# Optimization experiments

Hardware: AMD Instinct MI355X
Metric: run time of the kernel (lower is better)

## Reference

```python
import jax, jax.numpy as jnp
import numpy as np

B, H, S, DK = 2, 16, 2048, 64


def setup_inputs() -> dict:
    key = jax.random.key(0)
    kq, kk, kv = jax.random.split(key, 3)
    query = jax.random.normal(kq, (B, H, S, DK), dtype=jnp.float32)
    k = jax.random.normal(kk, (B, H, S, DK), dtype=jnp.float32)
    value = jax.random.normal(kv, (B, H, S, DK), dtype=jnp.float32)
    # causal padding-style mask: 1 = keep, 0 = masked (set to -inf pre-softmax)
    mask = jnp.tril(jnp.ones((S, S), dtype=jnp.int32))[None, None, :, :]
    return {"query": query, "key": k, "value": value, "d_k": DK, "mask": mask}


def reference(query, key, value, d_k, mask):
    # scores: [B, H, Sq, Sk]
    scores = jnp.einsum("bhqd,bhkd->bhqk", query, key)
    scores = scores / jnp.sqrt(jnp.asarray(d_k, dtype=scores.dtype))
    scores = jnp.where(mask == 0, -jnp.inf, scores)
    att = jax.nn.softmax(scores, axis=-1)
    # dropout is identity in eval mode (deterministic reference)
    out = jnp.einsum("bhqk,bhkd->bhqd", att, value)
    return out
```

## Files before the change

### kernel.cpp

```cpp
#include <hip/hip_runtime.h>
#include <cstdint>

#define B_ 2
#define H_ 16
#define S_ 2048
#define DK_ 64
#define BH_ (B_*H_)
#define NQT 32

typedef __attribute__((ext_vector_type(8))) short short8;
typedef __attribute__((ext_vector_type(4))) short short4v;
typedef __attribute__((ext_vector_type(4))) float floatx4;

__device__ inline unsigned short f2bf(float f) {
  union { float f; unsigned u; } v; v.f = f;
  unsigned u = v.u;
  unsigned r = u + 0x7fffu + ((u >> 16) & 1u);
  return (unsigned short)(r >> 16);
}

__device__ inline floatx4 mfma16(short4v a, short4v b, floatx4 c) {
#if __has_builtin(__builtin_amdgcn_mfma_f32_16x16x16bf16_1k)
  return __builtin_amdgcn_mfma_f32_16x16x16bf16_1k(a, b, c, 0, 0, 0);
#else
  asm("v_mfma_f32_16x16x16_bf16 %0, %1, %2, %0" : "+v"(c) : "v"(a), "v"(b));
  return c;
#endif
}

__device__ inline short4v u2s4(unsigned a, unsigned b) {
  union { unsigned u[2]; short4v s; } v;
  v.u[0] = a; v.u[1] = b;
  return v.s;
}

__global__ __launch_bounds__(256) void conv_kv(const float* __restrict__ K,
                                               const float* __restrict__ V,
                                               unsigned short* __restrict__ Kb,
                                               unsigned short* __restrict__ Vb) {
  __shared__ __align__(16) unsigned short t[64 * 80];
  const int bh = blockIdx.y, s0 = blockIdx.x * 64;
  const int row = threadIdx.x >> 2, cp = threadIdx.x & 3;

  {
    const float* src = K + ((size_t)(bh * S_ + s0 + row)) * DK_ + cp * 16;
    unsigned short* dst = Kb + ((size_t)(bh * S_ + s0 + row)) * DK_ + cp * 16;
    #pragma unroll
    for (int h = 0; h < 2; ++h) {
      float4 a = *(const float4*)(src + h * 8);
      float4 b = *(const float4*)(src + h * 8 + 4);
      uint4 st;
      st.x = (unsigned)f2bf(a.x) | ((unsigned)f2bf(a.y) << 16);
      st.y = (unsigned)f2bf(a.z) | ((unsigned)f2bf(a.w) << 16);
      st.z = (unsigned)f2bf(b.x) | ((unsigned)f2bf(b.y) << 16);
      st.w = (unsigned)f2bf(b.z) | ((unsigned)f2bf(b.w) << 16);
      *(uint4*)(dst + h * 8) = st;
    }
  }
  {
    const float* src = V + ((size_t)(bh * S_ + s0 + row)) * DK_ + cp * 16;
    #pragma unroll
    for (int j4 = 0; j4 < 4; ++j4) {
      float4 a = *(const float4*)(src + j4 * 4);
      int c = cp * 16 + j4 * 4;
      t[(c + 0) * 80 + row] = f2bf(a.x);
      t[(c + 1) * 80 + row] = f2bf(a.y);
      t[(c + 2) * 80 + row] = f2bf(a.z);
      t[(c + 3) * 80 + row] = f2bf(a.w);
    }
    __syncthreads();
    unsigned short* dst = Vb + ((size_t)(bh * DK_ + row)) * S_ + s0 + cp * 16;
    #pragma unroll
    for (int g = 0; g < 2; ++g) {
      const int pg = 2 * cp + g;
      const int t2r = pg >> 2, q = pg & 3;
      uint2 a = *(const uint2*)&t[row * 80 + 32 * t2r + 4 * q];
      uint2 b = *(const uint2*)&t[row * 80 + 32 * t2r + 16 + 4 * q];
      uint4 st = {a.x, a.y, b.x, b.y};
      *(uint4*)(dst + g * 8) = st;
    }
  }
}

__global__ __launch_bounds__(256, 2)
void fa_kernel(const float* __restrict__ Q, const unsigned short* __restrict__ Kb,
               const unsigned short* __restrict__ Vb, float* __restrict__ Out) {
  __shared__ __align__(16) unsigned short Kt[8192];
  __shared__ __align__(16) unsigned short Vt[8192];

  const int tid  = threadIdx.x;
  const int wave = tid >> 6;
  const int lane = tid & 63;
  const int quad = lane >> 4;
  const int l16  = lane & 15;
  const int wq   = wave & 1;
  const int ws   = wave >> 1;

  const int id = blockIdx.x;
  const int bh = (id & 7) | (((id >> 3) & 3) << 3);
  const int qt = NQT - 1 - (id >> 5);

  const float SCL = 0.125f * 1.44269504088896340736f;

  short8 qf[4];
  #pragma unroll
  for (int nq = 0; nq < 2; ++nq) {
    const float* p = Q + ((size_t)bh * S_ + qt * 64 + wq * 32 + nq * 16 + l16) * DK_ + quad * 8;
    #pragma unroll
    for (int ks = 0; ks < 2; ++ks) {
      float4 x = *(const float4*)(p + ks * 32);
      float4 y = *(const float4*)(p + ks * 32 + 4);
      short8 t;
      t[0]=(short)f2bf(x.x*SCL); t[1]=(short)f2bf(x.y*SCL); t[2]=(short)f2bf(x.z*SCL); t[3]=(short)f2bf(x.w*SCL);
      t[4]=(short)f2bf(y.x*SCL); t[5]=(short)f2bf(y.y*SCL); t[6]=(short)f2bf(y.z*SCL); t[7]=(short)f2bf(y.w*SCL);
      qf[nq * 2 + ks] = t;
    }
  }

  floatx4 Ot[4][2];
  float ls[2] = {0.f, 0.f};
  #pragma unroll
  for (int d = 0; d < 4; ++d)
    #pragma unroll
    for (int nq = 0; nq < 2; ++nq) Ot[d][nq] = (floatx4){0,0,0,0};

  const int nkv = (qt >> 1) + 1;
  for (int kv = 0; kv < nkv; ++kv) {
    if (kv) __syncthreads();
    #pragma unroll
    for (int rd = 0; rd < 4; ++rd) {
      const int cid = rd * 256 + wave * 64 + lane;
      {
        int row = cid >> 3, p = cid & 7, c = p ^ (row & 7);
        const unsigned short* g = Kb + (((size_t)bh * S_ + kv * 128 + row) << 6) + (c << 3);
        __builtin_amdgcn_global_load_lds(
            (const __attribute__((address_space(1))) void*)g,
            (__attribute__((address_space(3))) void*)&Kt[(rd * 4 + wave) * 512], 16, 0, 0);
      }
      {
        int row = cid >> 4, p = cid & 15, c = p ^ (row & 15);
        const unsigned short* g = Vb + (((size_t)bh * DK_ + row) << 11) + kv * 128 + (c << 3);
        __builtin_amdgcn_global_load_lds(
            (const __attribute__((address_space(1))) void*)g,
            (__attribute__((address_space(3))) void*)&Vt[(rd * 4 + wave) * 512], 16, 0, 0);
      }
    }
    __syncthreads();

    const bool domask = (kv == nkv - 1);
    unsigned pk[4][2][2];
    #pragma unroll
    for (int nt = 0; nt < 4; ++nt) {
      const int row = ws * 64 + nt * 16 + l16;
      floatx4 s0 = (floatx4){0,0,0,0}, s1 = (floatx4){0,0,0,0};
      #pragma unroll
      for (int ks = 0; ks < 2; ++ks) {
        const int p = (ks * 4 + quad) ^ (row & 7);
        const short8 ak = *(const short8*)&Kt[row * 64 + p * 8];
        s0 = __builtin_amdgcn_mfma_f32_16x16x32_bf16(ak, qf[ks],     s0, 0, 0, 0);
        s1 = __builtin_amdgcn_mfma_f32_16x16x32_bf16(ak, qf[2 + ks], s1, 0, 0, 0);
      }
      if (domask) {
        const int sb  = kv * 128 + ws * 64 + nt * 16 + quad * 4;
        const int q0r = qt * 64 + wq * 32 + l16;
        #pragma unroll
        for (int r = 0; r < 4; ++r) {
          if (sb + r > q0r)      s0[r] = -INFINITY;
          if (sb + r > q0r + 16) s1[r] = -INFINITY;
        }
      }
      #pragma unroll
      for (int nq = 0; nq < 2; ++nq) {
        const floatx4 sv = nq ? s1 : s0;
        float e0 = __builtin_amdgcn_exp2f(sv[0]);
        float e1 = __builtin_amdgcn_exp2f(sv[1]);
        float e2 = __builtin_amdgcn_exp2f(sv[2]);
        float e3 = __builtin_amdgcn_exp2f(sv[3]);
        ls[nq] += (e0 + e1) + (e2 + e3);
        pk[nt][nq][0] = __builtin_amdgcn_perm(__float_as_uint(e1) + 0x8000u,
                                              __float_as_uint(e0) + 0x8000u, 0x07060302u);
        pk[nt][nq][1] = __builtin_amdgcn_perm(__float_as_uint(e3) + 0x8000u,
                                              __float_as_uint(e2) + 0x8000u, 0x07060302u);
      }
    }
    #pragma unroll
    for (int dblk = 0; dblk < 4; ++dblk) {
      const int row = dblk * 16 + l16;
      #pragma unroll
      for (int tt = 0; tt < 2; ++tt) {
        const int p = ((ws * 2 + tt) * 4 + quad) ^ l16;
        const short8 v8 = *(const short8*)&Vt[row * 128 + p * 8];
        const short4v vlo = __builtin_shufflevector(v8, v8, 0, 1, 2, 3);
        const short4v vhi = __builtin_shufflevector(v8, v8, 4, 5, 6, 7);
        #pragma unroll
        for (int nq = 0; nq < 2; ++nq) {
          Ot[dblk][nq] = mfma16(vlo, u2s4(pk[2*tt  ][nq][0], pk[2*tt  ][nq][1]), Ot[dblk][nq]);
          Ot[dblk][nq] = mfma16(vhi, u2s4(pk[2*tt+1][nq][0], pk[2*tt+1][nq][1]), Ot[dblk][nq]);
        }
      }
    }
  }
  __syncthreads();

  #pragma unroll
  for (int nq = 0; nq < 2; ++nq) {
    ls[nq] += __shfl_xor(ls[nq], 16);
    ls[nq] += __shfl_xor(ls[nq], 32);
  }
  float* OP = (float*)&Kt[0];
  float* LP = (float*)&Vt[0];
  if (ws == 1) {
    #pragma unroll
    for (int nq = 0; nq < 2; ++nq) {
      const int rowi = (wq * 2 + nq) * 16 + l16;
      #pragma unroll
      for (int dblk = 0; dblk < 4; ++dblk) {
        const int c2 = (dblk * 4 + quad) ^ (l16 & 12);
        *(floatx4*)&OP[rowi * 64 + c2 * 4] = Ot[dblk][nq];
      }
      if (quad == 0) LP[rowi] = ls[nq];
    }
  }
  __syncthreads();
  if (ws == 0) {
    #pragma unroll
    for (int nq = 0; nq < 2; ++nq) {
      const int rowi = (wq * 2 + nq) * 16 + l16;
      const float inv = 1.0f / (ls[nq] + LP[rowi]);
      float* og = Out + ((size_t)bh * S_ + qt * 64 + wq * 32 + nq * 16 + l16) * DK_;
      #pragma unroll
      for (int dblk = 0; dblk < 4; ++dblk) {
        const int c2 = (dblk * 4 + quad) ^ (l16 & 12);
        floatx4 tot = Ot[dblk][nq] + *(const floatx4*)&OP[rowi * 64 + c2 * 4];
        tot *= inv;
        *(floatx4*)(og + dblk * 16 + quad * 4) = tot;
      }
    }
  }
}

extern "C" void kernel_launch(void* const* d_in, const int* in_sizes, int n_in,
                              void* d_out, int out_size, void* d_ws, size_t ws_size,
                              hipStream_t stream) {
  const float* Q = (const float*)d_in[0];
  const float* K = (const float*)d_in[1];
  const float* V = (const float*)d_in[2];
  float* Out = (float*)d_out;
  unsigned short* Kb = (unsigned short*)d_ws;
  unsigned short* Vb = Kb + (size_t)BH_ * S_ * DK_;
  conv_kv<<<dim3(S_ / 64, BH_), 256, 0, stream>>>(K, V, Kb, Vb);
  fa_kernel<<<dim3(NQT * BH_), 256, 0, stream>>>(Q, Kb, Vb, Out);
}
```

Before: 140.6 us.

## Replace 4-wave LDS-tiled attention blocks with single-wave blocks reading K/V directly

Each block becomes one wavefront handling a 32-row query strip, loading K and V fragments straight from global memory instead of staging 128-key tiles into shared memory. This removes the LDS staging, the barriers and the cross-wave reduction of partial outputs. The grid grows to 2048 small blocks for finer load balancing across the causal workload. In exchange K/V reuse across query waves now depends on L2/L1 caching, and there is no prefetch overlap.

```diff
diff --git a/kernel.cpp b/kernel.cpp
--- a/kernel.cpp
+++ b/kernel.cpp
@@ -6,7 +6,6 @@
 #define S_ 2048
 #define DK_ 64
 #define BH_ (B_*H_)
-#define NQT 32
 
 typedef __attribute__((ext_vector_type(8))) short short8;
 typedef __attribute__((ext_vector_type(4))) short short4v;
@@ -82,30 +81,22 @@
   }
 }
 
-__global__ __launch_bounds__(256, 2)
+__global__ __launch_bounds__(64, 3)
 void fa_kernel(const float* __restrict__ Q, const unsigned short* __restrict__ Kb,
                const unsigned short* __restrict__ Vb, float* __restrict__ Out) {
-  __shared__ __align__(16) unsigned short Kt[8192];
-  __shared__ __align__(16) unsigned short Vt[8192];
-
-  const int tid  = threadIdx.x;
-  const int wave = tid >> 6;
-  const int lane = tid & 63;
+  const int lane = threadIdx.x;
   const int quad = lane >> 4;
   const int l16  = lane & 15;
-  const int wq   = wave & 1;
-  const int ws   = wave >> 1;
-
-  const int id = blockIdx.x;
-  const int bh = (id & 7) | (((id >> 3) & 3) << 3);
-  const int qt = NQT - 1 - (id >> 5);
+  const int id   = blockIdx.x;
+  const int bh   = id & 31;
+  const int strip = 63 - (id >> 5);
 
   const float SCL = 0.125f * 1.44269504088896340736f;
 
   short8 qf[4];
   #pragma unroll
   for (int nq = 0; nq < 2; ++nq) {
-    const float* p = Q + ((size_t)bh * S_ + qt * 64 + wq * 32 + nq * 16 + l16) * DK_ + quad * 8;
+    const float* p = Q + ((size_t)bh * S_ + strip * 32 + nq * 16 + l16) * DK_ + quad * 8;
     #pragma unroll
     for (int ks = 0; ks < 2; ++ks) {
       float4 x = *(const float4*)(p + ks * 32);
@@ -124,54 +115,37 @@
     #pragma unroll
     for (int nq = 0; nq < 2; ++nq) Ot[d][nq] = (floatx4){0,0,0,0};
 
-  const int nkv = (qt >> 1) + 1;
-  for (int kv = 0; kv < nkv; ++kv) {
-    if (kv) __syncthreads();
-    #pragma unroll
-    for (int rd = 0; rd < 4; ++rd) {
-      const int cid = rd * 256 + wave * 64 + lane;
-      {
-        int row = cid >> 3, p = cid & 7, c = p ^ (row & 7);
-        const unsigned short* g = Kb + (((size_t)bh * S_ + kv * 128 + row) << 6) + (c << 3);
-        __builtin_amdgcn_global_load_lds(
-            (const __attribute__((address_space(1))) void*)g,
-            (__attribute__((address_space(3))) void*)&Kt[(rd * 4 + wave) * 512], 16, 0, 0);
-      }
-      {
-        int row = cid >> 4, p = cid & 15, c = p ^ (row & 15);
-        const unsigned short* g = Vb + (((size_t)bh * DK_ + row) << 11) + kv * 128 + (c << 3);
-        __builtin_amdgcn_global_load_lds(
-            (const __attribute__((address_space(1))) void*)g,
-            (__attribute__((address_space(3))) void*)&Vt[(rd * 4 + wave) * 512], 16, 0, 0);
-      }
-    }
-    __syncthreads();
-
-    const bool domask = (kv == nkv - 1);
+  const unsigned short* Kbase = Kb + (size_t)bh * S_ * DK_;
+  const unsigned short* Vbase = Vb + (size_t)bh * DK_ * S_;
+
+  const int niter = (strip >> 1) + 1;
+
+  for (int it = 0; it < niter; ++it) {
+    const int s0 = it * 64;
+    const bool dm = (it == niter - 1);
     unsigned pk[4][2][2];
+
     #pragma unroll
     for (int nt = 0; nt < 4; ++nt) {
-      const int row = ws * 64 + nt * 16 + l16;
-      floatx4 s0 = (floatx4){0,0,0,0}, s1 = (floatx4){0,0,0,0};
+      floatx4 a0 = (floatx4){0,0,0,0}, a1 = (floatx4){0,0,0,0};
       #pragma unroll
       for (int ks = 0; ks < 2; ++ks) {
-        const int p = (ks * 4 + quad) ^ (row & 7);
-        const short8 ak = *(const short8*)&Kt[row * 64 + p * 8];
-        s0 = __builtin_amdgcn_mfma_f32_16x16x32_bf16(ak, qf[ks],     s0, 0, 0, 0);
-        s1 = __builtin_amdgcn_mfma_f32_16x16x32_bf16(ak, qf[2 + ks], s1, 0, 0, 0);
-      }
-      if (domask) {
-        const int sb  = kv * 128 + ws * 64 + nt * 16 + quad * 4;
-        const int q0r = qt * 64 + wq * 32 + l16;
+        const short8 kf = *(const short8*)(Kbase + (size_t)(s0 + nt * 16 + l16) * DK_ + ks * 32 + quad * 8);
+        a0 = __builtin_amdgcn_mfma_f32_16x16x32_bf16(kf, qf[ks],     a0, 0, 0, 0);
+        a1 = __builtin_amdgcn_mfma_f32_16x16x32_bf16(kf, qf[2 + ks], a1, 0, 0, 0);
+      }
+      if (dm) {
+        const int sg = s0 + nt * 16 + quad * 4;
+        const int q0 = strip * 32 + l16;
         #pragma unroll
         for (int r = 0; r < 4; ++r) {
-          if (sb + r > q0r)      s0[r] = -INFINITY;
-          if (sb + r > q0r + 16) s1[r] = -INFINITY;
+          if (sg + r > q0)      a0[r] = -INFINITY;
+          if (sg + r > q0 + 16) a1[r] = -INFINITY;
         }
       }
       #pragma unroll
       for (int nq = 0; nq < 2; ++nq) {
-        const floatx4 sv = nq ? s1 : s0;
+        const floatx4 sv = nq ? a1 : a0;
         float e0 = __builtin_amdgcn_exp2f(sv[0]);
         float e1 = __builtin_amdgcn_exp2f(sv[1]);
         float e2 = __builtin_amdgcn_exp2f(sv[2]);
@@ -183,13 +157,13 @@
                                               __float_as_uint(e2) + 0x8000u, 0x07060302u);
       }
     }
+
     #pragma unroll
     for (int dblk = 0; dblk < 4; ++dblk) {
-      const int row = dblk * 16 + l16;
+      const unsigned short* vp = Vbase + (size_t)(dblk * 16 + l16) * S_ + s0 + quad * 8;
       #pragma unroll
       for (int tt = 0; tt < 2; ++tt) {
-        const int p = ((ws * 2 + tt) * 4 + quad) ^ l16;
-        const short8 v8 = *(const short8*)&Vt[row * 128 + p * 8];
+        const short8 v8 = *(const short8*)(vp + tt * 32);
         const short4v vlo = __builtin_shufflevector(v8, v8, 0, 1, 2, 3);
         const short4v vhi = __builtin_shufflevector(v8, v8, 4, 5, 6, 7);
         #pragma unroll
@@ -200,41 +174,20 @@
       }
     }
   }
-  __syncthreads();
 
   #pragma unroll
   for (int nq = 0; nq < 2; ++nq) {
     ls[nq] += __shfl_xor(ls[nq], 16);
     ls[nq] += __shfl_xor(ls[nq], 32);
   }
-  float* OP = (float*)&Kt[0];
-  float* LP = (float*)&Vt[0];
-  if (ws == 1) {
-    #pragma unroll
-    for (int nq = 0; nq < 2; ++nq) {
-      const int rowi = (wq * 2 + nq) * 16 + l16;
-      #pragma unroll
-      for (int dblk = 0; dblk < 4; ++dblk) {
-        const int c2 = (dblk * 4 + quad) ^ (l16 & 12);
-        *(floatx4*)&OP[rowi * 64 + c2 * 4] = Ot[dblk][nq];
-      }
-      if (quad == 0) LP[rowi] = ls[nq];
-    }
-  }
-  __syncthreads();
-  if (ws == 0) {
-    #pragma unroll
-    for (int nq = 0; nq < 2; ++nq) {
-      const int rowi = (wq * 2 + nq) * 16 + l16;
-      const float inv = 1.0f / (ls[nq] + LP[rowi]);
-      float* og = Out + ((size_t)bh * S_ + qt * 64 + wq * 32 + nq * 16 + l16) * DK_;
-      #pragma unroll
-      for (int dblk = 0; dblk < 4; ++dblk) {
-        const int c2 = (dblk * 4 + quad) ^ (l16 & 12);
-        floatx4 tot = Ot[dblk][nq] + *(const floatx4*)&OP[rowi * 64 + c2 * 4];
-        tot *= inv;
-        *(floatx4*)(og + dblk * 16 + quad * 4) = tot;
-      }
+  #pragma unroll
+  for (int nq = 0; nq < 2; ++nq) {
+    const float inv = 1.0f / ls[nq];
+    float* og = Out + ((size_t)bh * S_ + strip * 32 + nq * 16 + l16) * DK_;
+    #pragma unroll
+    for (int dblk = 0; dblk < 4; ++dblk) {
+      floatx4 tot = Ot[dblk][nq] * inv;
+      *(floatx4*)(og + dblk * 16 + quad * 4) = tot;
     }
   }
 }
@@ -249,5 +202,5 @@
   unsigned short* Kb = (unsigned short*)d_ws;
   unsigned short* Vb = Kb + (size_t)BH_ * S_ * DK_;
   conv_kv<<<dim3(S_ / 64, BH_), 256, 0, stream>>>(K, V, Kb, Vb);
-  fa_kernel<<<dim3(NQT * BH_), 256, 0, stream>>>(Q, Kb, Vb, Out);
-}
+  fa_kernel<<<dim3(64 * BH_), 64, 0, stream>>>(Q, Kb, Vb, Out);
+}
```

New measurement: 207.0 us. +47.2%, slower.

## Double-buffer K tiles in LDS and load V fragments directly into registers

Applied to the files above, without the earlier changes.

K tiles are now double-buffered in shared memory, and the next tile is prefetched asynchronously while the current one is computed, so each iteration needs only one barrier. V no longer goes through shared memory. Each wave reads its V fragments straight from global memory into registers at the start of the iteration. This hides load latency behind the MFMA work, at the cost of more registers and uncoalesced 16-byte global V loads that are exposed if the cache misses.

```diff
diff --git a/kernel.cpp b/kernel.cpp
--- a/kernel.cpp
+++ b/kernel.cpp
@@ -85,8 +85,7 @@
 __global__ __launch_bounds__(256, 2)
 void fa_kernel(const float* __restrict__ Q, const unsigned short* __restrict__ Kb,
                const unsigned short* __restrict__ Vb, float* __restrict__ Out) {
-  __shared__ __align__(16) unsigned short Kt[8192];
-  __shared__ __align__(16) unsigned short Vt[8192];
+  __shared__ __align__(16) unsigned short Kt[2][8192];
 
   const int tid  = threadIdx.x;
   const int wave = tid >> 6;
@@ -124,54 +123,69 @@
     #pragma unroll
     for (int nq = 0; nq < 2; ++nq) Ot[d][nq] = (floatx4){0,0,0,0};
 
+  const unsigned short* Kbase = Kb + (size_t)bh * S_ * DK_;
+  const unsigned short* Vbase = Vb + (size_t)bh * DK_ * S_ + ws * 64 + quad * 8;
+
+  int lofs[4];
+  #pragma unroll
+  for (int rd = 0; rd < 4; ++rd) {
+    const int cid = rd * 256 + wave * 64 + lane;
+    const int row = cid >> 3, p = cid & 7, c = p ^ (row & 7);
+    lofs[rd] = row * 64 + c * 8;
+  }
+
+  auto stageK = [&](int buf, int kv) {
+    #pragma unroll
+    for (int rd = 0; rd < 4; ++rd) {
+      const unsigned short* g = Kbase + kv * (128 * DK_) + lofs[rd];
+      __builtin_amdgcn_global_load_lds(
+          (const __attribute__((address_space(1))) void*)g,
+          (__attribute__((address_space(3))) void*)&Kt[buf][(rd * 4 + wave) * 512], 16, 0, 0);
+    }
+  };
+
   const int nkv = (qt >> 1) + 1;
+  stageK(0, 0);
+  __syncthreads();
+
+  int cur = 0;
   for (int kv = 0; kv < nkv; ++kv) {
-    if (kv) __syncthreads();
-    #pragma unroll
-    for (int rd = 0; rd < 4; ++rd) {
-      const int cid = rd * 256 + wave * 64 + lane;
-      {
-        int row = cid >> 3, p = cid & 7, c = p ^ (row & 7);
-        const unsigned short* g = Kb + (((size_t)bh * S_ + kv * 128 + row) << 6) + (c << 3);
-        __builtin_amdgcn_global_load_lds(
-            (const __attribute__((address_space(1))) void*)g,
-            (__attribute__((address_space(3))) void*)&Kt[(rd * 4 + wave) * 512], 16, 0, 0);
-      }
-      {
-        int row = cid >> 4, p = cid & 15, c = p ^ (row & 15);
-        const unsigned short* g = Vb + (((size_t)bh * DK_ + row) << 11) + kv * 128 + (c << 3);
-        __builtin_amdgcn_global_load_lds(
-            (const __attribute__((address_space(1))) void*)g,
-            (__attribute__((address_space(3))) void*)&Vt[(rd * 4 + wave) * 512], 16, 0, 0);
-      }
-    }
-    __syncthreads();
-
-    const bool domask = (kv == nkv - 1);
+    const int s0 = kv * 128;
+    const bool dm = (kv == nkv - 1);
+
+    short8 v8[4][2];
+    #pragma unroll
+    for (int dblk = 0; dblk < 4; ++dblk)
+      #pragma unroll
+      for (int tt = 0; tt < 2; ++tt)
+        v8[dblk][tt] = *(const short8*)(Vbase + (size_t)(dblk * 16 + l16) * S_ + s0 + tt * 32);
+
+    if (kv + 1 < nkv) stageK(cur ^ 1, kv + 1);
+
     unsigned pk[4][2][2];
     #pragma unroll
     for (int nt = 0; nt < 4; ++nt) {
       const int row = ws * 64 + nt * 16 + l16;
-      floatx4 s0 = (floatx4){0,0,0,0}, s1 = (floatx4){0,0,0,0};
+      floatx4 a0 = (floatx4){0,0,0,0}, a1 = (floatx4){0,0,0,0};
       #pragma unroll
       for (int ks = 0; ks < 2; ++ks) {
         const int p = (ks * 4 + quad) ^ (row & 7);
-        const short8 ak = *(const short8*)&Kt[row * 64 + p * 8];
-        s0 = __builtin_amdgcn_mfma_f32_16x16x32_bf16(ak, qf[ks],     s0, 0, 0, 0);
-        s1 = __builtin_amdgcn_mfma_f32_16x16x32_bf16(ak, qf[2 + ks], s1, 0, 0, 0);
-      }
-      if (domask) {
-        const int sb  = kv * 128 + ws * 64 + nt * 16 + quad * 4;
-        const int q0r = qt * 64 + wq * 32 + l16;
+        const short8 ak = *(const short8*)&Kt[cur][row * 64 + p * 8];
+        a0 = __builtin_amdgcn_mfma_f32_16x16x32_bf16(ak, qf[ks],     a0, 0, 0, 0);
+        a1 = __builtin_amdgcn_mfma_f32_16x16x32_bf16(ak, qf[2 + ks], a1, 0, 0, 0);
+      }
+      if (dm) {
+        const int sg = s0 + ws * 64 + nt * 16 + quad * 4;
+        const int q0 = qt * 64 + wq * 32 + l16;
         #pragma unroll
         for (int r = 0; r < 4; ++r) {
-          if (sb + r > q0r)      s0[r] = -INFINITY;
-          if (sb + r > q0r + 16) s1[r] = -INFINITY;
+          if (sg + r > q0)      a0[r] = -INFINITY;
+          if (sg + r > q0 + 16) a1[r] = -INFINITY;
         }
       }
       #pragma unroll
       for (int nq = 0; nq < 2; ++nq) {
-        const floatx4 sv = nq ? s1 : s0;
+        const floatx4 sv = nq ? a1 : a0;
         float e0 = __builtin_amdgcn_exp2f(sv[0]);
         float e1 = __builtin_amdgcn_exp2f(sv[1]);
         float e2 = __builtin_amdgcn_exp2f(sv[2]);
@@ -183,15 +197,14 @@
                                               __float_as_uint(e2) + 0x8000u, 0x07060302u);
       }
     }
+
     #pragma unroll
     for (int dblk = 0; dblk < 4; ++dblk) {
-      const int row = dblk * 16 + l16;
       #pragma unroll
       for (int tt = 0; tt < 2; ++tt) {
-        const int p = ((ws * 2 + tt) * 4 + quad) ^ l16;
-        const short8 v8 = *(const short8*)&Vt[row * 128 + p * 8];
-        const short4v vlo = __builtin_shufflevector(v8, v8, 0, 1, 2, 3);
-        const short4v vhi = __builtin_shufflevector(v8, v8, 4, 5, 6, 7);
+        const short8 vv = v8[dblk][tt];
+        const short4v vlo = __builtin_shufflevector(vv, vv, 0, 1, 2, 3);
+        const short4v vhi = __builtin_shufflevector(vv, vv, 4, 5, 6, 7);
         #pragma unroll
         for (int nq = 0; nq < 2; ++nq) {
           Ot[dblk][nq] = mfma16(vlo, u2s4(pk[2*tt  ][nq][0], pk[2*tt  ][nq][1]), Ot[dblk][nq]);
@@ -199,16 +212,18 @@
         }
       }
     }
-  }
-  __syncthreads();
+
+    __syncthreads();
+    cur ^= 1;
+  }
 
   #pragma unroll
   for (int nq = 0; nq < 2; ++nq) {
     ls[nq] += __shfl_xor(ls[nq], 16);
     ls[nq] += __shfl_xor(ls[nq], 32);
   }
-  float* OP = (float*)&Kt[0];
-  float* LP = (float*)&Vt[0];
+  float* OP = (float*)&Kt[0][0];
+  float* LP = (float*)&Kt[1][0];
   if (ws == 1) {
     #pragma unroll
     for (int nq = 0; nq < 2; ++nq) {
```

New measurement: 149.0 us. 1.06x slower.
